# Optimization experiments

Measured on AMD Instinct MI355X. Metric: run time of the kernel, lower is better.

Reference implementation:

```python
import jax, jax.numpy as jnp
import numpy as np

BLOCK_SIZE = 11   # adaptive window (odd)
CONSTANT = 0.02   # subtracted from local mean (cv2 'C'), scaled for [0,1] images
MAXVAL = 1.0      # maxValue=1 in the original layer


def _local_mean(x, k):
    """Box-filter local mean with replicate border, matching cv2 BORDER_REPLICATE.
    x: [B, H, W] float32 -> [B, H, W] local means over k x k windows."""
    p = k // 2
    xp = jnp.pad(x, ((0, 0), (p, p), (p, p)), mode='edge')
    x4 = xp[:, None, :, :]                                   # [B,1,H+2p,W+2p] NCHW
    kern = jnp.full((1, 1, k, k), 1.0 / (k * k), dtype=x.dtype)  # OIHW
    mean = jax.lax.conv_general_dilated(
        x4, kern, window_strides=(1, 1), padding='VALID',
        dimension_numbers=('NCHW', 'OIHW', 'NCHW'))
    return mean[:, 0, :, :]


def setup_inputs() -> dict:
    key = jax.random.key(0)
    input_batch = jax.random.uniform(key, (128, 512, 512), dtype=jnp.float32)
    return {"input_batch": input_batch}


def reference(input_batch) -> jnp.ndarray:
    # cv2.adaptiveThreshold(..., ADAPTIVE_THRESH_MEAN_C, THRESH_BINARY_INV, blockSize, C):
    #   T(x,y) = mean_{kxk window}(src) - C
    #   dst = maxValue if src <= T else 0   (BINARY_INV)
    thresh = _local_mean(input_batch, BLOCK_SIZE) - CONSTANT   # [B,H,W]
    return jnp.where(input_batch > thresh, 0.0, MAXVAL).astype(jnp.float32)
```

## Files before the change

kernel.cpp:

```cpp
#include <hip/hip_runtime.h>


#define IMG_W 512
#define IMG_H 512
#define TLX 64
#define TLY 32
#define HALO 5
#define RWX (TLX + 2 * HALO)
#define RWY (TLY + 2 * HALO)
#define RPAD 75
#define HPAD 65
#define NTHREADS 256
#define RUNX 16
#define RUNY 8
#define THRESH_INT (-20300431)

__global__ __launch_bounds__(NTHREADS, 6) void adaptive_thresh_kernel(
    const float* __restrict__ in, float* __restrict__ out) {
  __shared__ int raw[RWY * RPAD];
  __shared__ int hsum[RWY * HPAD];

  const int tid = threadIdx.x;
  const int bx0 = blockIdx.x * TLX;
  const int by0 = blockIdx.y * TLY;
  const size_t img_off = (size_t)blockIdx.z * (IMG_W * IMG_H);
  const float* img = in + img_off;
  float* oimg = out + img_off;

  for (int p = tid; p < RWY * RWX; p += NTHREADS) {
    int r = p / RWX, c = p - r * RWX;
    int gy = min(max(by0 - HALO + r, 0), IMG_H - 1);
    int gx = min(max(bx0 - HALO + c, 0), IMG_W - 1);
    raw[r * RPAD + c] = (int)(img[gy * IMG_W + gx] * 8388608.0f);
  }
  __syncthreads();

  for (int t = tid; t < RWY * (TLX / RUNX); t += NTHREADS) {
    int r = t >> 2, x0 = (t & 3) * RUNX;
    const int* rp = &raw[r * RPAD + x0];
    int* hp = &hsum[r * HPAD + x0];
    int s = 0;
#pragma unroll
    for (int d = 0; d < 11; ++d) s += rp[d];
    hp[0] = s;
#pragma unroll
    for (int i = 1; i < RUNX; ++i) {
      s += rp[10 + i] - rp[i - 1];
      hp[i] = s;
    }
  }
  __syncthreads();

  {
    const int x = tid & 63;
    const int y0 = (tid >> 6) * RUNY;
    int s = 0;
#pragma unroll
    for (int d = 0; d < 11; ++d) s += hsum[(y0 + d) * HPAD + x];
#pragma unroll
    for (int i = 0; i < RUNY; ++i) {
      if (i) s += hsum[(y0 + 10 + i) * HPAD + x] - hsum[(y0 + i - 1) * HPAD + x];
      int iv = raw[(y0 + i + HALO) * RPAD + (x + HALO)];
      oimg[(size_t)(by0 + y0 + i) * IMG_W + (bx0 + x)] =
          (121 * iv - s >= THRESH_INT) ? 0.0f : 1.0f;
    }
  }
}

extern "C" void kernel_launch(void* const* d_in, const int* in_sizes, int n_in,
                              void* d_out, int out_size, void* d_ws, size_t ws_size,
                              hipStream_t stream) {
  const float* in = (const float*)d_in[0];
  float* out = (float*)d_out;
  dim3 grid(IMG_W / TLX, IMG_H / TLY, 128);
  dim3 block(NTHREADS);
  adaptive_thresh_kernel<<<grid, block, 0, stream>>>(in, out);
}
```

Before: 279.9 us.

## Vectorize box-filter threshold kernel with float4 I/O and taller tiles

Tile height doubles to 64 rows, which cuts halo overhead. Interior tiles now load the input with aligned float4 reads over an 84-wide window. The horizontal and vertical passes and the output stores use int4/float4 shared-memory accesses and register arrays. The goal is fewer memory instructions and better coalescing in a bandwidth-bound stencil. In exchange the shared footprint grows, more registers are used per thread, and the launch bounds hint is gone, so occupancy may drop.

```diff
diff --git a/kernel.cpp b/kernel.cpp
--- a/kernel.cpp
+++ b/kernel.cpp
@@ -4,65 +4,99 @@
 #define IMG_W 512
 #define IMG_H 512
 #define TLX 64
-#define TLY 32
+#define TLY 64
 #define HALO 5
-#define RWX (TLX + 2 * HALO)
 #define RWY (TLY + 2 * HALO)
-#define RPAD 75
-#define HPAD 65
+#define RPADQ 21
+#define HPADQ 17
 #define NTHREADS 256
-#define RUNX 16
-#define RUNY 8
 #define THRESH_INT (-20300431)
 
-__global__ __launch_bounds__(NTHREADS, 6) void adaptive_thresh_kernel(
-    const float* __restrict__ in, float* __restrict__ out) {
-  __shared__ int raw[RWY * RPAD];
-  __shared__ int hsum[RWY * HPAD];
+__global__ void adaptive_thresh_kernel(const float* __restrict__ in,
+                                       float* __restrict__ out) {
+  __shared__ alignas(16) int4 raw4[RWY * RPADQ];
+  __shared__ alignas(16) int4 hsum4[RWY * HPADQ];
 
   const int tid = threadIdx.x;
-  const int bx0 = blockIdx.x * TLX;
-  const int by0 = blockIdx.y * TLY;
+  const int bx = blockIdx.x;
+  const int bx0 = bx * TLX, by0 = blockIdx.y * TLY;
   const size_t img_off = (size_t)blockIdx.z * (IMG_W * IMG_H);
   const float* img = in + img_off;
   float* oimg = out + img_off;
+  int* raw = (int*)raw4;
 
-  for (int p = tid; p < RWY * RWX; p += NTHREADS) {
-    int r = p / RWX, c = p - r * RWX;
-    int gy = min(max(by0 - HALO + r, 0), IMG_H - 1);
-    int gx = min(max(bx0 - HALO + c, 0), IMG_W - 1);
-    raw[r * RPAD + c] = (int)(img[gy * IMG_W + gx] * 8388608.0f);
-  }
-  __syncthreads();
-
-  for (int t = tid; t < RWY * (TLX / RUNX); t += NTHREADS) {
-    int r = t >> 2, x0 = (t & 3) * RUNX;
-    const int* rp = &raw[r * RPAD + x0];
-    int* hp = &hsum[r * HPAD + x0];
-    int s = 0;
-#pragma unroll
-    for (int d = 0; d < 11; ++d) s += rp[d];
-    hp[0] = s;
-#pragma unroll
-    for (int i = 1; i < RUNX; ++i) {
-      s += rp[10 + i] - rp[i - 1];
-      hp[i] = s;
+  if (bx > 0 && bx < (IMG_W / TLX) - 1) {
+    for (int t = tid; t < RWY * RPADQ; t += NTHREADS) {
+      int r = (int)((unsigned)t / RPADQ);
+      int q = t - r * RPADQ;
+      int gy = min(max(by0 - HALO + r, 0), IMG_H - 1);
+      const float4 v = *(const float4*)&img[gy * IMG_W + (bx0 - 8) + 4 * q];
+      int4 iv;
+      iv.x = (int)(v.x * 8388608.0f);
+      iv.y = (int)(v.y * 8388608.0f);
+      iv.z = (int)(v.z * 8388608.0f);
+      iv.w = (int)(v.w * 8388608.0f);
+      raw4[r * RPADQ + q] = iv;
+    }
+  } else {
+    for (int p = tid; p < RWY * (RPADQ * 4); p += NTHREADS) {
+      int r = (int)((unsigned)p / (RPADQ * 4));
+      int c = p - r * (RPADQ * 4);
+      int gy = min(max(by0 - HALO + r, 0), IMG_H - 1);
+      int gx = min(max(bx0 - 8 + c, 0), IMG_W - 1);
+      raw[r * (RPADQ * 4) + c] = (int)(img[gy * IMG_W + gx] * 8388608.0f);
     }
   }
   __syncthreads();
 
-  {
-    const int x = tid & 63;
-    const int y0 = (tid >> 6) * RUNY;
+  for (int t = tid; t < RWY * 4; t += NTHREADS) {
+    int r = t >> 2, xq = t & 3;
+    const int4* rp = &raw4[r * RPADQ + 4 * xq];
+    int w[32];
+#pragma unroll
+    for (int k = 0; k < 8; ++k) {
+      int4 a = rp[k];
+      w[4 * k + 0] = a.x; w[4 * k + 1] = a.y;
+      w[4 * k + 2] = a.z; w[4 * k + 3] = a.w;
+    }
     int s = 0;
 #pragma unroll
-    for (int d = 0; d < 11; ++d) s += hsum[(y0 + d) * HPAD + x];
+    for (int m = 3; m <= 13; ++m) s += w[m];
+    int h[16];
+    h[0] = s;
 #pragma unroll
-    for (int i = 0; i < RUNY; ++i) {
-      if (i) s += hsum[(y0 + 10 + i) * HPAD + x] - hsum[(y0 + i - 1) * HPAD + x];
-      int iv = raw[(y0 + i + HALO) * RPAD + (x + HALO)];
-      oimg[(size_t)(by0 + y0 + i) * IMG_W + (bx0 + x)] =
-          (121 * iv - s >= THRESH_INT) ? 0.0f : 1.0f;
+    for (int j = 1; j < 16; ++j) { s += w[13 + j] - w[2 + j]; h[j] = s; }
+    int4* hp = &hsum4[r * HPADQ + 4 * xq];
+#pragma unroll
+    for (int k = 0; k < 4; ++k)
+      hp[k] = make_int4(h[4 * k], h[4 * k + 1], h[4 * k + 2], h[4 * k + 3]);
+  }
+  __syncthreads();
+
+  {
+    const int xg = tid & 15;
+    const int y0 = (tid >> 4) * 4;
+    int4 s = make_int4(0, 0, 0, 0);
+#pragma unroll
+    for (int d = 0; d < 11; ++d) {
+      int4 h = hsum4[(y0 + d) * HPADQ + xg];
+      s.x += h.x; s.y += h.y; s.z += h.z; s.w += h.w;
+    }
+#pragma unroll
+    for (int i = 0; i < 4; ++i) {
+      if (i) {
+        int4 hn = hsum4[(y0 + 10 + i) * HPADQ + xg];
+        int4 ho = hsum4[(y0 + i - 1) * HPADQ + xg];
+        s.x += hn.x - ho.x; s.y += hn.y - ho.y;
+        s.z += hn.z - ho.z; s.w += hn.w - ho.w;
+      }
+      int4 iv = raw4[(y0 + i + HALO) * RPADQ + 2 + xg];
+      float4 o;
+      o.x = (121 * iv.x - s.x >= THRESH_INT) ? 0.0f : 1.0f;
+      o.y = (121 * iv.y - s.y >= THRESH_INT) ? 0.0f : 1.0f;
+      o.z = (121 * iv.z - s.z >= THRESH_INT) ? 0.0f : 1.0f;
+      o.w = (121 * iv.w - s.w >= THRESH_INT) ? 0.0f : 1.0f;
+      *(float4*)&oimg[(size_t)(by0 + y0 + i) * IMG_W + bx0 + 4 * xg] = o;
     }
   }
 }
```

Result: faster. 257.2 us (-8.1%).
